# Kernel optimization log

Measured on AMD Instinct MI355X. Metric: run time of the kernel, lower is better.

The kernel has to match this reference:

```python
import jax, jax.numpy as jnp
import numpy as np

N, E, G = 20000, 160000, 64
IN_FULL, X_START, X_END = 16, 4, 10
H, OUT, RH, NE, K = 512, 512, 128, 4, 2
NL = 3               # GraphConv layers per expert
SPS, STEMP = 0.3, 1.0  # size_prior_strength, size_temperature


def setup_inputs() -> dict:
    key = jax.random.key(0)
    ks = jax.random.split(key, 10)
    def w(k, shape, fan):
        return jax.random.normal(k, shape, jnp.float32) / np.float32(np.sqrt(fan))
    return dict(
        x=jax.random.normal(ks[0], (N, IN_FULL), jnp.float32),
        edge_index=jax.random.randint(ks[1], (2, E), 0, N),
        batch=jnp.sort(jax.random.randint(ks[2], (N,), 0, G)),
        num_graphs=G,
        enc_W1=w(ks[3], (X_END - X_START, H), X_END - X_START), enc_b1=jnp.zeros((H,), jnp.float32),
        enc_W2=w(ks[4], (H, H), H), enc_b2=jnp.zeros((H,), jnp.float32),
        r_W1=w(ks[5], (H + 2, RH), H + 2), r_b1=jnp.zeros((RH,), jnp.float32),
        ln_g=jnp.ones((RH,), jnp.float32), ln_b=jnp.zeros((RH,), jnp.float32),
        r_W2=w(ks[6], (RH, NE), RH), r_b2=jnp.zeros((NE,), jnp.float32),
        size_centers=jnp.linspace(0.0, 1.0, NE).astype(jnp.float32),
        W_rel=w(ks[7], (NE, NL, H, H), H),       # GraphConv lin_rel weights (stacked)
        b_rel=jnp.zeros((NE, NL, H), jnp.float32),
        W_root=w(ks[8], (NE, NL, H, H), H),      # GraphConv lin_root weights (no bias)
    )


def reference(x, edge_index, batch, num_graphs, enc_W1, enc_b1, enc_W2, enc_b2,
              r_W1, r_b1, ln_g, ln_b, r_W2, r_b2, size_centers, W_rel, b_rel, W_root):
    src, dst = edge_index[0], edge_index[1]
    # encoder: Linear -> ReLU -> Linear on sliced node features
    h = jax.nn.relu(x[:, X_START:X_END] @ enc_W1 + enc_b1) @ enc_W2 + enc_b2
    # per-graph size features (log_nodes_edges mode)
    nodes = jnp.maximum(jax.ops.segment_sum(jnp.ones((N,), x.dtype), batch, num_segments=num_graphs), 1.0)
    edges = jax.ops.segment_sum(jnp.ones((E,), x.dtype), batch[src], num_segments=num_graphs)
    log_n, log_e = jnp.log(nodes), jnp.log1p(edges)
    f = jnp.stack([log_n, log_e], axis=-1)
    f = (f - f.mean(0, keepdims=True)) / (f.std(0, keepdims=True) + 1e-6)
    size_norm = (log_n - log_n.min()) / (log_n.max() - log_n.min() + 1e-6)
    # router: Linear -> LayerNorm -> ReLU -> Linear, plus size prior
    r = jnp.concatenate([h, f[batch]], axis=-1) @ r_W1 + r_b1
    r = (r - r.mean(-1, keepdims=True)) / jnp.sqrt(r.var(-1, keepdims=True) + 1e-5) * ln_g + ln_b
    logits = jax.nn.relu(r) @ r_W2 + r_b2
    prior = -(size_norm[batch][:, None] - size_centers[None, :]) ** 2 / STEMP
    logits = (1.0 - SPS) * logits + SPS * prior
    probs = jax.nn.softmax(logits, axis=-1)
    # top-k sparse gating, renormalized
    v, ix = jax.lax.top_k(probs, K)
    v = v / (v.sum(-1, keepdims=True) + 1e-8)
    weights = jnp.zeros_like(probs).at[jnp.arange(N)[:, None], ix].set(v)  # [N, NE]
    # GraphConv: out_i = (sum_{j->i} z_j) @ W_rel + b_rel + z_i @ W_root
    def gconv(z, Wr, br, Wo):
        agg = jax.ops.segment_sum(z[src], dst, num_segments=N)
        return agg @ Wr + br + z @ Wo
    out = jnp.zeros((N, OUT), x.dtype)
    for e in range(NE):  # small fixed expert count
        z = jax.nn.relu(gconv(h, W_rel[e, 0], b_rel[e, 0], W_root[e, 0]))
        z = jax.nn.relu(gconv(z, W_rel[e, 1], b_rel[e, 1], W_root[e, 1]))
        z = gconv(z, W_rel[e, 2], b_rel[e, 2], W_root[e, 2])
        out = out + weights[:, e:e + 1] * z
    return out
```

## Files before the change

### kernel.cpp

```cpp
#include <hip/hip_runtime.h>
#include <math.h>

#define N_NODES 20000
#define N_EDGES 160000
#define G_GRAPHS 64
#define H_DIM 512
#define RH_DIM 128
#define NE_EXP 4
#define P_ROWS 20096
#define EH_BLOCKS 64
#define WSZ (512 * 512)

typedef __attribute__((ext_vector_type(8))) short bf16x8;
typedef __attribute__((ext_vector_type(4))) float f32x4;

__device__ __forceinline__ ushort f2bf(float f) {
    uint u = __float_as_uint(f);
    return (ushort)((u + 0x7FFFu + ((u >> 16) & 1u)) >> 16);
}
__device__ __forceinline__ float bf2f(ushort h) {
    return __uint_as_float(((uint)h) << 16);
}

__device__ __forceinline__ void async_copy16(const void* g, void* l) {
    __builtin_amdgcn_global_load_lds(
        (__attribute__((address_space(1))) void*)g,
        (__attribute__((address_space(3))) void*)l, 16, 0, 0);
}

__device__ __forceinline__ int xcd_swizzle(int orig, int nwg) {
    const int q = nwg >> 3, r = nwg & 7;
    const int xcd = orig & 7, sid = orig >> 3;
    return (xcd < r ? xcd * (q + 1) : r * (q + 1) + (xcd - r) * q) + sid;
}

template<bool RELU, int EPI, int NE2>
__global__ __launch_bounds__(256)
void gemm_grp(const ushort* __restrict__ A1, size_t a1es,
              const ushort* __restrict__ W1, size_t w1es,
              const ushort* __restrict__ A2, size_t a2es,
              const ushort* __restrict__ W2, size_t w2es,
              const float* __restrict__ bias, size_t bes,
              const float* __restrict__ wcol,
              ushort* __restrict__ out0, size_t oes)
{
    __shared__ char smem[32768];
    const int tid = threadIdx.x;
    const int w = tid >> 6, lane = tid & 63;

    const int wgid = xcd_swizzle(blockIdx.x, gridDim.x);
    const int m0 = (wgid / (4 * NE2)) * 128;
    const int rem = wgid % (4 * NE2);
    const int e  = rem % NE2;
    const int n0 = (rem / NE2) * 128;

    const ushort* __restrict__ A1e = A1 + (size_t)e * a1es;
    const ushort* __restrict__ W1e = W1 + (size_t)e * w1es;
    const ushort* __restrict__ A2e = A2 + (size_t)e * a2es;
    const ushort* __restrict__ W2e = W2 + (size_t)e * w2es;
    const float*  __restrict__ be  = bias + (size_t)e * bes;
    ushort* __restrict__ oe = out0 + (size_t)e * oes;

    f32x4 acc[4][4];
#pragma unroll
    for (int i = 0; i < 4; ++i)
#pragma unroll
        for (int j = 0; j < 4; ++j) acc[i][j] = (f32x4){0.f, 0.f, 0.f, 0.f};

    const int srow = lane >> 2, schk = lane & 3;
    const int wr = w >> 1, wc = w & 1;
    const int row16 = lane & 15;
    const uint koffB = (uint)(lane >> 4) * 16u;
    const uint aoff0 = (uint)(wr * 64 + row16) * 64u + koffB;
    const uint boff0 = 8192u + (uint)(wc * 64 + row16) * 64u + koffB;

    auto stage = [&](int buf, int t) {
        const ushort* __restrict__ A  = (t < 16) ? A1e : A2e;
        const ushort* __restrict__ Wt = (t < 16) ? W1e : W2e;
        const int kt = (t & 15) * 32;
        char* base = smem + buf * 16384;
#pragma unroll
        for (int c = 0; c < 2; ++c) {
            const int rb = c * 64 + w * 16;
            async_copy16(A  + (size_t)(m0 + rb + srow) * 512 + kt + schk * 8, base + rb * 64);
            async_copy16(Wt + (size_t)(n0 + rb + srow) * 512 + kt + schk * 8, base + 8192 + rb * 64);
        }
    };
    auto compute = [&](int buf) {
        const char* base = smem + buf * 16384;
        bf16x8 af[4], bfr[4];
#pragma unroll
        for (int i = 0; i < 4; ++i) af[i] = *(const bf16x8*)(base + aoff0 + i * 1024);
#pragma unroll
        for (int j = 0; j < 4; ++j) bfr[j] = *(const bf16x8*)(base + boff0 + j * 1024);
#pragma unroll
        for (int i = 0; i < 4; ++i)
#pragma unroll
            for (int j = 0; j < 4; ++j)
                acc[i][j] = __builtin_amdgcn_mfma_f32_16x16x32_bf16(af[i], bfr[j], acc[i][j], 0, 0, 0);
    };

    stage(0, 0);
    for (int t = 0; t < 31; ++t) {
        stage((t + 1) & 1, t + 1);
        asm volatile("s_waitcnt vmcnt(4)" ::: "memory");
        __builtin_amdgcn_s_barrier();
        compute(t & 1);
        __builtin_amdgcn_s_barrier();
    }
    asm volatile("s_waitcnt vmcnt(0)" ::: "memory");
    __builtin_amdgcn_s_barrier();
    compute(1);

#pragma unroll
    for (int i = 0; i < 4; ++i) {
        const int r0 = m0 + wr * 64 + i * 16 + (lane >> 4) * 4;
#pragma unroll
        for (int j = 0; j < 4; ++j) {
            const int c = n0 + wc * 64 + j * 16 + row16;
            const float bj = be[c];
#pragma unroll
            for (int q2 = 0; q2 < 4; ++q2) {
                const int r = r0 + q2;
                float v = acc[i][j][q2] + bj;
                if (EPI == 0) {
                    if (RELU) v = fmaxf(v, 0.f);
                    oe[(size_t)r * 512 + c] = f2bf(v);
                } else {
                    const float wrow = (r < N_NODES) ? wcol[(size_t)r * 4 + e] : 0.f;
                    oe[(size_t)r * 512 + c] = f2bf(v * wrow);
                }
            }
        }
    }
}

template<int NPASS, int EPI, int NBN>
__global__ __launch_bounds__(256)
void gemm_mfma(const ushort* __restrict__ A0, const ushort* __restrict__ W0,
               const ushort* __restrict__ A1p, const ushort* __restrict__ W1p,
               const ushort* __restrict__ A2p, const ushort* __restrict__ W2p,
               const float* __restrict__ bias,
               void* __restrict__ out0, void* __restrict__ out1, int Ncols)
{
    __shared__ char smem[32768];
    const int tid = threadIdx.x;
    const int w = tid >> 6, lane = tid & 63;

    const int wgid = xcd_swizzle(blockIdx.x, gridDim.x);
    const int m0 = (wgid / NBN) * 128;
    const int n0 = (wgid % NBN) * 128;

    f32x4 acc[4][4];
#pragma unroll
    for (int i = 0; i < 4; ++i)
#pragma unroll
        for (int j = 0; j < 4; ++j) acc[i][j] = (f32x4){0.f, 0.f, 0.f, 0.f};

    const int srow = lane >> 2, schk = lane & 3;
    const int wr = w >> 1, wc = w & 1;
    const int row16 = lane & 15;
    const uint koffB = (uint)(lane >> 4) * 16u;
    const uint aoff0 = (uint)(wr * 64 + row16) * 64u + koffB;
    const uint boff0 = 8192u + (uint)(wc * 64 + row16) * 64u + koffB;

    const int NT = NPASS * 16;
    auto Asel = [&](int t) -> const ushort* { return (t < 16) ? A0 : ((t < 32) ? A1p : A2p); };
    auto Wsel = [&](int t) -> const ushort* { return (t < 16) ? W0 : ((t < 32) ? W1p : W2p); };

    auto stage = [&](int buf, int t) {
        const ushort* __restrict__ A  = Asel(t);
        const ushort* __restrict__ Wt = Wsel(t);
        const int kt = (t & 15) * 32;
        char* base = smem + buf * 16384;
#pragma unroll
        for (int c = 0; c < 2; ++c) {
            const int rb = c * 64 + w * 16;
            async_copy16(A  + (size_t)(m0 + rb + srow) * 512 + kt + schk * 8, base + rb * 64);
            async_copy16(Wt + (size_t)(n0 + rb + srow) * 512 + kt + schk * 8, base + 8192 + rb * 64);
        }
    };
    auto compute = [&](int buf) {
        const char* base = smem + buf * 16384;
        bf16x8 af[4], bfr[4];
#pragma unroll
        for (int i = 0; i < 4; ++i) af[i] = *(const bf16x8*)(base + aoff0 + i * 1024);
#pragma unroll
        for (int j = 0; j < 4; ++j) bfr[j] = *(const bf16x8*)(base + boff0 + j * 1024);
#pragma unroll
        for (int i = 0; i < 4; ++i)
#pragma unroll
            for (int j = 0; j < 4; ++j)
                acc[i][j] = __builtin_amdgcn_mfma_f32_16x16x32_bf16(af[i], bfr[j], acc[i][j], 0, 0, 0);
    };

    stage(0, 0);
    for (int t = 0; t < NT - 1; ++t) {
        stage((t + 1) & 1, t + 1);
        asm volatile("s_waitcnt vmcnt(4)" ::: "memory");
        __builtin_amdgcn_s_barrier();
        compute(t & 1);
        __builtin_amdgcn_s_barrier();
    }
    asm volatile("s_waitcnt vmcnt(0)" ::: "memory");
    __builtin_amdgcn_s_barrier();
    compute((NT - 1) & 1);

#pragma unroll
    for (int i = 0; i < 4; ++i) {
        const int r0 = m0 + wr * 64 + i * 16 + (lane >> 4) * 4;
#pragma unroll
        for (int j = 0; j < 4; ++j) {
            const int c = n0 + wc * 64 + j * 16 + row16;
            const float bj = (EPI == 5) ? 0.f : bias[c];
#pragma unroll
            for (int q2 = 0; q2 < 4; ++q2) {
                const int r = r0 + q2;
                float v = acc[i][j][q2] + bj;
                if (EPI == 4) {
                    const ushort hi = f2bf(v);
                    const ushort lo = f2bf(v - bf2f(hi));
                    ((ushort*)out0)[(size_t)r * Ncols + c] = hi;
                    ((ushort*)out1)[(size_t)r * Ncols + c] = lo;
                } else {
                    ((float*)out0)[(size_t)r * Ncols + c] = v;
                }
            }
        }
    }
}

__global__ __launch_bounds__(256)
void reduce_wz_kernel(const uint* __restrict__ wz4, float2* __restrict__ out)
{
    const size_t idx = (size_t)blockIdx.x * 256 + threadIdx.x;
    const size_t es = (size_t)P_ROWS * 256;
    const uint a = wz4[idx], b = wz4[idx + es];
    const uint c = wz4[idx + 2 * es], d = wz4[idx + 3 * es];
    float lo = bf2f((ushort)(a & 0xffffu)) + bf2f((ushort)(b & 0xffffu))
             + bf2f((ushort)(c & 0xffffu)) + bf2f((ushort)(d & 0xffffu));
    float hi = bf2f((ushort)(a >> 16)) + bf2f((ushort)(b >> 16))
             + bf2f((ushort)(c >> 16)) + bf2f((ushort)(d >> 16));
    out[idx] = make_float2(lo, hi);
}

__global__ void encoder1_kernel(const float* __restrict__ x, const float* __restrict__ W1,
                                const float* __restrict__ b1,
                                ushort* __restrict__ t1hi, ushort* __restrict__ t1lo)
{
    const int idx = blockIdx.x * blockDim.x + threadIdx.x;
    if (idx >= P_ROWS * H_DIM) return;
    const int i = idx / H_DIM, j = idx - i * H_DIM;
    float v = 0.f;
    if (i < N_NODES) {
        const float* xr = &x[i * 16 + 4];
        v = b1[j];
#pragma unroll
        for (int k = 0; k < 6; ++k) v = fmaf(xr[k], W1[k * H_DIM + j], v);
        v = fmaxf(v, 0.f);
    }
    const ushort hi = f2bf(v);
    t1hi[idx] = hi;
    t1lo[idx] = f2bf(v - bf2f(hi));
}

__global__ void zero_ints_kernel(int* __restrict__ p, int n)
{
    const int idx = blockIdx.x * blockDim.x + threadIdx.x;
    if (idx < n) p[idx] = 0;
}

__global__ void graph_bounds_kernel(const int* __restrict__ batch, int* __restrict__ gstart)
{
    const int g = threadIdx.x;
    if (g > G_GRAPHS) return;
    int lo = 0, hi = N_NODES;
    while (lo < hi) {
        const int mid = (lo + hi) >> 1;
        if (batch[mid] < g) lo = mid + 1; else hi = mid;
    }
    gstart[g] = lo;
}

__global__ __launch_bounds__(256)
void edge_hist_kernel(const int* __restrict__ src, const int* __restrict__ dst,
                      const int* __restrict__ batch,
                      int* __restrict__ part, int* __restrict__ deg)
{
    __shared__ int hist[G_GRAPHS];
    const int tid = threadIdx.x;
    if (tid < G_GRAPHS) hist[tid] = 0;
    __syncthreads();
    for (int e = blockIdx.x * 256 + tid; e < N_EDGES; e += EH_BLOCKS * 256) {
        atomicAdd(&deg[dst[e]], 1);
        atomicAdd(&hist[batch[src[e]]], 1);
    }
    __syncthreads();
    if (tid < G_GRAPHS) part[blockIdx.x * G_GRAPHS + tid] = hist[tid];
}

__global__ void stats_finalize_kernel(const int* __restrict__ gstart, const int* __restrict__ part,
                                      float* __restrict__ f_norm, float* __restrict__ size_norm)
{
    const int g = threadIdx.x;
    const float nn = fmaxf((float)(gstart[g + 1] - gstart[g]), 1.0f);
    int ec = 0;
#pragma unroll 8
    for (int b = 0; b < EH_BLOCKS; ++b) ec += part[b * G_GRAPHS + g];
    const float ee = (float)ec;
    const float ln = logf(nn);
    const float le = log1pf(ee);
    float s0 = ln, s1 = le;
#pragma unroll
    for (int o = 32; o > 0; o >>= 1) { s0 += __shfl_xor(s0, o); s1 += __shfl_xor(s1, o); }
    const float m0 = s0 / 64.f, m1 = s1 / 64.f;
    const float d0 = ln - m0, d1 = le - m1;
    float v0 = d0 * d0, v1 = d1 * d1;
#pragma unroll
    for (int o = 32; o > 0; o >>= 1) { v0 += __shfl_xor(v0, o); v1 += __shfl_xor(v1, o); }
    const float sd0 = sqrtf(v0 / 64.f), sd1 = sqrtf(v1 / 64.f);
    float mn = ln, mx = ln;
#pragma unroll
    for (int o = 32; o > 0; o >>= 1) {
        mn = fminf(mn, __shfl_xor(mn, o));
        mx = fmaxf(mx, __shfl_xor(mx, o));
    }
    f_norm[g * 2 + 0] = d0 / (sd0 + 1e-6f);
    f_norm[g * 2 + 1] = d1 / (sd1 + 1e-6f);
    size_norm[g] = (ln - mn) / (mx - mn + 1e-6f);
}

__global__ void scan_kernel(const int* __restrict__ in, int* __restrict__ row_ptr,
                            int* __restrict__ cursor, int n)
{
    __shared__ int wsum[16];
    __shared__ int carry_s;
    const int tid = threadIdx.x;
    const int lane = tid & 63, wv = tid >> 6;
    if (tid == 0) carry_s = 0;
    __syncthreads();
    for (int base = 0; base < n; base += 1024) {
        const int idx = base + tid;
        const int v = (idx < n) ? in[idx] : 0;
        int x = v;
#pragma unroll
        for (int o = 1; o < 64; o <<= 1) { const int t = __shfl_up(x, o); if (lane >= o) x += t; }
        if (lane == 63) wsum[wv] = x;
        __syncthreads();
        const int carry = carry_s;
        if (wv == 0) {
            int y = (lane < 16) ? wsum[lane] : 0;
#pragma unroll
            for (int o = 1; o < 16; o <<= 1) { const int t = __shfl_up(y, o); if (lane >= o) y += t; }
            if (lane < 16) wsum[lane] = y;
        }
        __syncthreads();
        const int woff = (wv > 0) ? wsum[wv - 1] : 0;
        const int excl = x - v + woff + carry;
        if (idx < n) { row_ptr[idx] = excl; cursor[idx] = excl; }
        __syncthreads();
        if (tid == 0) carry_s = carry + wsum[15];
        __syncthreads();
    }
    if (tid == 0) row_ptr[n] = carry_s;
}

__global__ void scatter_kernel(const int* __restrict__ src, const int* __restrict__ dst,
                               int* __restrict__ cursor, int* __restrict__ csr_col)
{
    const int e = blockIdx.x * blockDim.x + threadIdx.x;
    if (e >= N_EDGES) return;
    const int d = dst[e];
    const int slot = atomicAdd(&cursor[d], 1);
    csr_col[slot] = src[e];
}

__global__ void sort_adj_kernel(const int* __restrict__ row_ptr, int* __restrict__ csr_col)
{
    const int i = blockIdx.x * blockDim.x + threadIdx.x;
    if (i >= N_NODES) return;
    const int b = row_ptr[i], e = row_ptr[i + 1];
    for (int p = b + 1; p < e; ++p) {
        const int key = csr_col[p];
        int q = p - 1;
        while (q >= b && csr_col[q] > key) { csr_col[q + 1] = csr_col[q]; --q; }
        csr_col[q + 1] = key;
    }
}

__global__ __launch_bounds__(256)
void aggregate_bf16(const uint4* __restrict__ z4, const int* __restrict__ row_ptr,
                    const int* __restrict__ csr_col, uint4* __restrict__ agg4)
{
    const size_t es = (size_t)blockIdx.y * P_ROWS * 64;
    const uint4* __restrict__ zz = z4 + es;
    uint4* __restrict__ aa = agg4 + es;
    const int i = blockIdx.x * 4 + (threadIdx.x >> 6);
    const int lane = threadIdx.x & 63;
    const int b = row_ptr[i], e = row_ptr[i + 1];
    float acc[8];
#pragma unroll
    for (int k = 0; k < 8; ++k) acc[k] = 0.f;
    auto add8 = [&](uint4 v) {
        acc[0] += bf2f((ushort)(v.x & 0xffffu)); acc[1] += bf2f((ushort)(v.x >> 16));
        acc[2] += bf2f((ushort)(v.y & 0xffffu)); acc[3] += bf2f((ushort)(v.y >> 16));
        acc[4] += bf2f((ushort)(v.z & 0xffffu)); acc[5] += bf2f((ushort)(v.z >> 16));
        acc[6] += bf2f((ushort)(v.w & 0xffffu)); acc[7] += bf2f((ushort)(v.w >> 16));
    };
    int p = b;
    for (; p + 2 <= e; p += 2) {
        const uint4 v0 = zz[(size_t)csr_col[p] * 64 + lane];
        const uint4 v1 = zz[(size_t)csr_col[p + 1] * 64 + lane];
        add8(v0);
        add8(v1);
    }
    if (p < e) add8(zz[(size_t)csr_col[p] * 64 + lane]);
    uint4 o;
    o.x = (uint)f2bf(acc[0]) | ((uint)f2bf(acc[1]) << 16);
    o.y = (uint)f2bf(acc[2]) | ((uint)f2bf(acc[3]) << 16);
    o.z = (uint)f2bf(acc[4]) | ((uint)f2bf(acc[5]) << 16);
    o.w = (uint)f2bf(acc[6]) | ((uint)f2bf(acc[7]) << 16);
    aa[(size_t)i * 64 + lane] = o;
}

__global__ __launch_bounds__(256)
void transpose_f32_to_bf16(const float* __restrict__ W, ushort* __restrict__ Wt)
{
    __shared__ float tile[32][33];
    const float* Wm = W + (size_t)blockIdx.z * WSZ;
    ushort* Wtm = Wt + (size_t)blockIdx.z * WSZ;
    const int c0 = blockIdx.x * 32, r0 = blockIdx.y * 32;
    const int tc = threadIdx.x & 31, tr = threadIdx.x >> 5;
#pragma unroll
    for (int it = 0; it < 4; ++it)
        tile[tr + it * 8][tc] = Wm[(size_t)(r0 + tr + it * 8) * 512 + c0 + tc];
    __syncthreads();
#pragma unroll
    for (int it = 0; it < 4; ++it) {
        const int cr = tr + it * 8;
        Wtm[(size_t)(c0 + cr) * 512 + r0 + tc] = f2bf(tile[tc][cr]);
    }
}

__global__ __launch_bounds__(256)
void transpose_split_kernel(const float* __restrict__ W, ushort* __restrict__ Whi,
                            ushort* __restrict__ Wlo, int Nin)
{
    __shared__ float tile[32][33];
    const int c0 = blockIdx.x * 32;
    const int r0 = blockIdx.y * 32;
    const int tc = threadIdx.x & 31, tr = threadIdx.x >> 5;
#pragma unroll
    for (int it = 0; it < 4; ++it)
        tile[tr + it * 8][tc] = W[(size_t)(r0 + tr + it * 8) * Nin + c0 + tc];
    __syncthreads();
#pragma unroll
    for (int it = 0; it < 4; ++it) {
        const int cr = tr + it * 8;
        const float v = tile[tc][cr];
        const ushort hi = f2bf(v);
        Whi[(size_t)(c0 + cr) * 512 + r0 + tc] = hi;
        Wlo[(size_t)(c0 + cr) * 512 + r0 + tc] = f2bf(v - bf2f(hi));
    }
}

__global__ __launch_bounds__(128)
void router_kernel(const float* __restrict__ rtmp, const int* __restrict__ batch,
                   const float* __restrict__ rW1, const float* __restrict__ rb1,
                   const float* __restrict__ lng, const float* __restrict__ lnb,
                   const float* __restrict__ rW2, const float* __restrict__ rb2,
                   const float* __restrict__ centers,
                   const float* __restrict__ f_norm, const float* __restrict__ size_norm,
                   float* __restrict__ weights)
{
    const int i = blockIdx.x;
    const int j = threadIdx.x;
    const int g = batch[i];
    const float f0 = f_norm[g * 2], f1 = f_norm[g * 2 + 1];
    float r = rtmp[(size_t)i * RH_DIM + j]
            + f0 * rW1[512 * RH_DIM + j] + f1 * rW1[513 * RH_DIM + j] + rb1[j];

    __shared__ float part[2];
    __shared__ float rbuf[RH_DIM];
    __shared__ float lbuf[4];
    const int lane = j & 63, wv = j >> 6;

    float s = r;
#pragma unroll
    for (int o = 32; o > 0; o >>= 1) s += __shfl_xor(s, o);
    if (lane == 0) part[wv] = s;
    __syncthreads();
    const float mean = (part[0] + part[1]) / 128.f;
    __syncthreads();
    const float d = r - mean;
    float v = d * d;
#pragma unroll
    for (int o = 32; o > 0; o >>= 1) v += __shfl_xor(v, o);
    if (lane == 0) part[wv] = v;
    __syncthreads();
    const float var = (part[0] + part[1]) / 128.f;
    const float rn = d / sqrtf(var + 1e-5f) * lng[j] + lnb[j];
    rbuf[j] = fmaxf(rn, 0.f);
    __syncthreads();

    if (j < 4) {
        float acc = rb2[j];
        for (int t = 0; t < RH_DIM; ++t) acc = fmaf(rbuf[t], rW2[t * 4 + j], acc);
        const float sn = size_norm[g];
        const float dd = sn - centers[j];
        lbuf[j] = 0.7f * acc + 0.3f * (-(dd * dd));
    }
    __syncthreads();
    if (j == 0) {
        float p[4];
        const float mx = fmaxf(fmaxf(lbuf[0], lbuf[1]), fmaxf(lbuf[2], lbuf[3]));
#pragma unroll
        for (int c = 0; c < 4; ++c) p[c] = expf(lbuf[c] - mx);
        const float ssum = p[0] + p[1] + p[2] + p[3];
#pragma unroll
        for (int c = 0; c < 4; ++c) p[c] /= ssum;
        int i1 = 0;
#pragma unroll
        for (int c = 1; c < 4; ++c) if (p[c] > p[i1]) i1 = c;
        int i2 = -1;
#pragma unroll
        for (int c = 0; c < 4; ++c) {
            if (c == i1) continue;
            if (i2 < 0 || p[c] > p[i2]) i2 = c;
        }
        const float vs = p[i1] + p[i2] + 1e-8f;
        float wout[4] = {0.f, 0.f, 0.f, 0.f};
        wout[i1] = p[i1] / vs;
        wout[i2] = p[i2] / vs;
#pragma unroll
        for (int c = 0; c < 4; ++c) weights[(size_t)i * 4 + c] = wout[c];
    }
}

extern "C" void kernel_launch(void* const* d_in, const int* in_sizes, int n_in,
                              void* d_out, int out_size, void* d_ws, size_t ws_size,
                              hipStream_t stream)
{
    const float* x       = (const float*)d_in[0];
    const int*   ei      = (const int*)d_in[1];
    const int*   batch   = (const int*)d_in[2];
    const float* enc_W1  = (const float*)d_in[4];
    const float* enc_b1  = (const float*)d_in[5];
    const float* enc_W2  = (const float*)d_in[6];
    const float* enc_b2  = (const float*)d_in[7];
    const float* r_W1    = (const float*)d_in[8];
    const float* r_b1    = (const float*)d_in[9];
    const float* ln_g    = (const float*)d_in[10];
    const float* ln_b    = (const float*)d_in[11];
    const float* r_W2    = (const float*)d_in[12];
    const float* r_b2    = (const float*)d_in[13];
    const float* centers = (const float*)d_in[14];
    const float* W_rel   = (const float*)d_in[15];
    const float* b_rel   = (const float*)d_in[16];
    const float* W_root  = (const float*)d_in[17];
    const int* src = ei;
    const int* dst = ei + N_EDGES;
    float* out = (float*)d_out;

    const size_t PF = (size_t)P_ROWS * H_DIM;
    const size_t PF2 = PF * 2;

    char* wsp = (char*)d_ws;
    size_t off = 0;
    auto alloc = [&](size_t bytes) -> char* {
        char* p = wsp + off;
        off = (off + bytes + 255) & ~(size_t)255;
        return p;
    };
    char* region1 = alloc(PF * 4);
    ushort* t1hi = (ushort*)region1;
    ushort* t1lo = (ushort*)(region1 + PF * 2);
    ushort* wz4  = (ushort*)region1;
    char* region2 = alloc(PF * 4);
    ushort* h_hi = (ushort*)region2;
    ushort* h_lo = (ushort*)(region2 + PF * 2);
    char* B_zA = alloc(PF2 * 2);
    ushort* zAe = (ushort*)B_zA;
    float*  rtmp = (float*)B_zA;
    char* B_zB = alloc(PF2 * 2);
    ushort* zBe = (ushort*)B_zB;
    char* B_ag = alloc(PF2 * 2);
    ushort* agge = (ushort*)B_ag;
    ushort* aggH16 = (ushort*)alloc(PF * 2);
    ushort* Wt_rel16  = (ushort*)alloc((size_t)12 * WSZ * 2);
    ushort* Wt_root16 = (ushort*)alloc((size_t)12 * WSZ * 2);
    ushort* W2t_hi = (ushort*)alloc((size_t)WSZ * 2);
    ushort* W2t_lo = (ushort*)alloc((size_t)WSZ * 2);
    ushort* rW1t_hi = (ushort*)alloc((size_t)128 * 512 * 2);
    ushort* rW1t_lo = (ushort*)alloc((size_t)128 * 512 * 2);
    float*  weights = (float*)alloc((size_t)P_ROWS * 4 * 4);
    int* deg     = (int*)alloc((size_t)N_NODES * 4);
    int* gstart  = (int*)alloc((size_t)(G_GRAPHS + 1) * 4);
    int* part    = (int*)alloc((size_t)EH_BLOCKS * G_GRAPHS * 4);
    int* row_ptr = (int*)alloc((size_t)(N_NODES + 1) * 4);
    int* cursor  = (int*)alloc((size_t)N_NODES * 4);
    int* csr_col = (int*)alloc((size_t)N_EDGES * 4);
    float* f_norm    = (float*)alloc((size_t)G_GRAPHS * 2 * 4);
    float* size_norm = (float*)alloc((size_t)G_GRAPHS * 4);
    (void)in_sizes; (void)n_in; (void)out_size; (void)ws_size;

    const int enc_nwg  = 4 * (P_ROWS / 128);
    const int rtr_nwg  = 1 * (P_ROWS / 128);
    const int grp_nwg2 = 8 * (P_ROWS / 128);
    const dim3 tr_grid(16, 16, 12);
    const dim3 agg_grid1(N_NODES / 4, 1);
    const dim3 agg_grid2(N_NODES / 4, 2);

    zero_ints_kernel<<<(N_NODES + 255) / 256, 256, 0, stream>>>(deg, N_NODES);
    transpose_f32_to_bf16<<<tr_grid, 256, 0, stream>>>(W_rel, Wt_rel16);
    transpose_f32_to_bf16<<<tr_grid, 256, 0, stream>>>(W_root, Wt_root16);
    transpose_split_kernel<<<dim3(16, 16), 256, 0, stream>>>(enc_W2, W2t_hi, W2t_lo, 512);
    transpose_split_kernel<<<dim3(4, 16), 256, 0, stream>>>(r_W1, rW1t_hi, rW1t_lo, 128);
    graph_bounds_kernel<<<1, 128, 0, stream>>>(batch, gstart);
    edge_hist_kernel<<<EH_BLOCKS, 256, 0, stream>>>(src, dst, batch, part, deg);
    stats_finalize_kernel<<<1, 64, 0, stream>>>(gstart, part, f_norm, size_norm);
    encoder1_kernel<<<(P_ROWS * H_DIM + 255) / 256, 256, 0, stream>>>(x, enc_W1, enc_b1, t1hi, t1lo);
    gemm_mfma<3, 4, 4><<<enc_nwg, 256, 0, stream>>>(
        t1hi, W2t_hi, t1hi, W2t_lo, t1lo, W2t_hi, enc_b2, h_hi, h_lo, 512);
    gemm_mfma<3, 5, 1><<<rtr_nwg, 256, 0, stream>>>(
        h_hi, rW1t_hi, h_hi, rW1t_lo, h_lo, rW1t_hi, nullptr, rtmp, nullptr, 128);
    router_kernel<<<N_NODES, 128, 0, stream>>>(rtmp, batch, r_W1, r_b1, ln_g, ln_b,
                                               r_W2, r_b2, centers, f_norm, size_norm, weights);
    scan_kernel<<<1, 1024, 0, stream>>>(deg, row_ptr, cursor, N_NODES);
    scatter_kernel<<<(N_EDGES + 255) / 256, 256, 0, stream>>>(src, dst, cursor, csr_col);
    sort_adj_kernel<<<(N_NODES + 255) / 256, 256, 0, stream>>>(row_ptr, csr_col);
    aggregate_bf16<<<agg_grid1, 256, 0, stream>>>((const uint4*)h_hi, row_ptr, csr_col,
                                                  (uint4*)aggH16);

    const size_t WES = (size_t)3 * WSZ;
    const size_t BES = (size_t)3 * 512;
    for (int p = 0; p < 2; ++p) {
        const size_t eb = (size_t)(p * 2);
        const ushort* WrP = Wt_rel16  + eb * WES;
        const ushort* WoP = Wt_root16 + eb * WES;
        const float*  brP = b_rel + eb * BES;
        ushort* wzP = wz4 + eb * PF;
        gemm_grp<true, 0, 2><<<grp_nwg2, 256, 0, stream>>>(
            aggH16, 0, WrP, WES, h_hi, 0, WoP, WES, brP, BES, nullptr, zAe, PF);
        aggregate_bf16<<<agg_grid2, 256, 0, stream>>>((const uint4*)zAe, row_ptr, csr_col,
                                                      (uint4*)agge);
        gemm_grp<true, 0, 2><<<grp_nwg2, 256, 0, stream>>>(
            agge, PF, WrP + WSZ, WES, zAe, PF, WoP + WSZ, WES, brP + 512, BES, nullptr, zBe, PF);
        aggregate_bf16<<<agg_grid2, 256, 0, stream>>>((const uint4*)zBe, row_ptr, csr_col,
                                                      (uint4*)agge);
        gemm_grp<false, 6, 2><<<grp_nwg2, 256, 0, stream>>>(
            agge, PF, WrP + 2 * WSZ, WES, zBe, PF, WoP + 2 * WSZ, WES, brP + 1024, BES,
            weights + eb, wzP, PF);
    }
    reduce_wz_kernel<<<N_NODES, 256, 0, stream>>>((const uint*)wz4, (float2*)out);
}
```

Baseline: 837.5 us.

## Compute last GraphConv layer only for rows routed to each expert

```diff
diff --git a/kernel.cpp b/kernel.cpp
--- a/kernel.cpp
+++ b/kernel.cpp
@@ -34,14 +34,13 @@
     return (xcd < r ? xcd * (q + 1) : r * (q + 1) + (xcd - r) * q) + sid;
 }
 
-template<bool RELU, int EPI, int NE2>
+template<bool RELU, int NE2>
 __global__ __launch_bounds__(256)
 void gemm_grp(const ushort* __restrict__ A1, size_t a1es,
               const ushort* __restrict__ W1, size_t w1es,
               const ushort* __restrict__ A2, size_t a2es,
               const ushort* __restrict__ W2, size_t w2es,
               const float* __restrict__ bias, size_t bes,
-              const float* __restrict__ wcol,
               ushort* __restrict__ out0, size_t oes)
 {
     __shared__ char smem[32768];
@@ -121,15 +120,120 @@
             const float bj = be[c];
 #pragma unroll
             for (int q2 = 0; q2 < 4; ++q2) {
-                const int r = r0 + q2;
                 float v = acc[i][j][q2] + bj;
-                if (EPI == 0) {
-                    if (RELU) v = fmaxf(v, 0.f);
-                    oe[(size_t)r * 512 + c] = f2bf(v);
-                } else {
-                    const float wrow = (r < N_NODES) ? wcol[(size_t)r * 4 + e] : 0.f;
-                    oe[(size_t)r * 512 + c] = f2bf(v * wrow);
-                }
+                if (RELU) v = fmaxf(v, 0.f);
+                oe[(size_t)(r0 + q2) * 512 + c] = f2bf(v);
+            }
+        }
+    }
+}
+
+__global__ __launch_bounds__(256)
+void gemm_l2(const ushort* __restrict__ A1, size_t a1es,
+             const ushort* __restrict__ W1, size_t w1es,
+             const ushort* __restrict__ A2, size_t a2es,
+             const ushort* __restrict__ W2, size_t w2es,
+             const float* __restrict__ bias, size_t bes,
+             const float* __restrict__ weights4,
+             const int* __restrict__ lists, const int* __restrict__ cnt8,
+             int egbase, ushort* __restrict__ planes)
+{
+    __shared__ char smem[32768];
+    const int tid = threadIdx.x;
+    const int w = tid >> 6, lane = tid & 63;
+
+    const int wgid = xcd_swizzle(blockIdx.x, gridDim.x);
+    const int m0 = (wgid / 16) * 128;
+    const int rem = wgid % 16;
+    const int li = rem & 3;
+    const int n0 = (rem >> 2) * 128;
+    const int el = li >> 1, pl = li & 1;
+    const int eg = egbase + el;
+    const int lid = eg * 2 + pl;
+    const int cnt = cnt8[lid];
+    if (m0 >= cnt) return;
+    const int* __restrict__ idxl = lists + (size_t)lid * N_NODES;
+
+    const ushort* __restrict__ A1e = A1 + (size_t)el * a1es;
+    const ushort* __restrict__ W1e = W1 + (size_t)el * w1es;
+    const ushort* __restrict__ A2e = A2 + (size_t)el * a2es;
+    const ushort* __restrict__ W2e = W2 + (size_t)el * w2es;
+    const float*  __restrict__ be  = bias + (size_t)el * bes;
+
+    f32x4 acc[4][4];
+#pragma unroll
+    for (int i = 0; i < 4; ++i)
+#pragma unroll
+        for (int j = 0; j < 4; ++j) acc[i][j] = (f32x4){0.f, 0.f, 0.f, 0.f};
+
+    const int srow = lane >> 2, schk = lane & 3;
+    const int wr = w >> 1, wc = w & 1;
+    const int row16 = lane & 15;
+    const uint koffB = (uint)(lane >> 4) * 16u;
+    const uint aoff0 = (uint)(wr * 64 + row16) * 64u + koffB;
+    const uint boff0 = 8192u + (uint)(wc * 64 + row16) * 64u + koffB;
+
+    size_t arow[2];
+#pragma unroll
+    for (int c = 0; c < 2; ++c) {
+        int slot = m0 + c * 64 + w * 16 + srow;
+        slot = (slot < cnt) ? slot : (cnt - 1);
+        arow[c] = (size_t)idxl[slot] * 512 + schk * 8;
+    }
+
+    auto stage = [&](int buf, int t) {
+        const ushort* __restrict__ A  = (t < 16) ? A1e : A2e;
+        const ushort* __restrict__ Wt = (t < 16) ? W1e : W2e;
+        const int kt = (t & 15) * 32;
+        char* base = smem + buf * 16384;
+#pragma unroll
+        for (int c = 0; c < 2; ++c) {
+            const int rb = c * 64 + w * 16;
+            async_copy16(A + arow[c] + kt, base + rb * 64);
+            async_copy16(Wt + (size_t)(n0 + rb + srow) * 512 + kt + schk * 8, base + 8192 + rb * 64);
+        }
+    };
+    auto compute = [&](int buf) {
+        const char* base = smem + buf * 16384;
+        bf16x8 af[4], bfr[4];
+#pragma unroll
+        for (int i = 0; i < 4; ++i) af[i] = *(const bf16x8*)(base + aoff0 + i * 1024);
+#pragma unroll
+        for (int j = 0; j < 4; ++j) bfr[j] = *(const bf16x8*)(base + boff0 + j * 1024);
+#pragma unroll
+        for (int i = 0; i < 4; ++i)
+#pragma unroll
+            for (int j = 0; j < 4; ++j)
+                acc[i][j] = __builtin_amdgcn_mfma_f32_16x16x32_bf16(af[i], bfr[j], acc[i][j], 0, 0, 0);
+    };
+
+    stage(0, 0);
+    for (int t = 0; t < 31; ++t) {
+        stage((t + 1) & 1, t + 1);
+        asm volatile("s_waitcnt vmcnt(4)" ::: "memory");
+        __builtin_amdgcn_s_barrier();
+        compute(t & 1);
+        __builtin_amdgcn_s_barrier();
+    }
+    asm volatile("s_waitcnt vmcnt(0)" ::: "memory");
+    __builtin_amdgcn_s_barrier();
+    compute(1);
+
+    ushort* __restrict__ plane = planes + (size_t)pl * ((size_t)P_ROWS * H_DIM);
+#pragma unroll
+    for (int i = 0; i < 4; ++i) {
+        const int s0 = m0 + wr * 64 + i * 16 + (lane >> 4) * 4;
+#pragma unroll
+        for (int q2 = 0; q2 < 4; ++q2) {
+            const int s = s0 + q2;
+            if (s >= cnt) continue;
+            const int r = idxl[s];
+            const float wrow = weights4[(size_t)r * 4 + eg];
+#pragma unroll
+            for (int j = 0; j < 4; ++j) {
+                const int c = n0 + wc * 64 + j * 16 + row16;
+                const float v = acc[i][j][q2] + be[c];
+                plane[(size_t)r * 512 + c] = f2bf(v * wrow);
             }
         }
     }
@@ -231,17 +335,44 @@
 }
 
 __global__ __launch_bounds__(256)
-void reduce_wz_kernel(const uint* __restrict__ wz4, float2* __restrict__ out)
+void reduce2_kernel(const uint* __restrict__ p0, const uint* __restrict__ p1,
+                    float2* __restrict__ out)
 {
     const size_t idx = (size_t)blockIdx.x * 256 + threadIdx.x;
-    const size_t es = (size_t)P_ROWS * 256;
-    const uint a = wz4[idx], b = wz4[idx + es];
-    const uint c = wz4[idx + 2 * es], d = wz4[idx + 3 * es];
-    float lo = bf2f((ushort)(a & 0xffffu)) + bf2f((ushort)(b & 0xffffu))
-             + bf2f((ushort)(c & 0xffffu)) + bf2f((ushort)(d & 0xffffu));
-    float hi = bf2f((ushort)(a >> 16)) + bf2f((ushort)(b >> 16))
-             + bf2f((ushort)(c >> 16)) + bf2f((ushort)(d >> 16));
+    const uint a = p0[idx], b = p1[idx];
+    float lo = bf2f((ushort)(a & 0xffffu)) + bf2f((ushort)(b & 0xffffu));
+    float hi = bf2f((ushort)(a >> 16)) + bf2f((ushort)(b >> 16));
     out[idx] = make_float2(lo, hi);
+}
+
+__global__ __launch_bounds__(256)
+void select_kernel(const float* __restrict__ weights, int* __restrict__ cnt8,
+                   int* __restrict__ lists)
+{
+    __shared__ int lcnt[8];
+    __shared__ int lbase[8];
+    const int tid = threadIdx.x;
+    if (tid < 8) lcnt[tid] = 0;
+    __syncthreads();
+    const int r = blockIdx.x * 256 + tid;
+    int e1 = -1, e2 = -1, s1 = 0, s2 = 0;
+    if (r < N_NODES) {
+#pragma unroll
+        for (int c = 0; c < 4; ++c) {
+            if (weights[(size_t)r * 4 + c] > 0.f) {
+                if (e1 < 0) e1 = c; else e2 = c;
+            }
+        }
+        s1 = atomicAdd(&lcnt[e1 * 2 + 0], 1);
+        s2 = atomicAdd(&lcnt[e2 * 2 + 1], 1);
+    }
+    __syncthreads();
+    if (tid < 8) lbase[tid] = atomicAdd(&cnt8[tid], lcnt[tid]);
+    __syncthreads();
+    if (r < N_NODES) {
+        lists[(size_t)(e1 * 2 + 0) * N_NODES + lbase[e1 * 2 + 0] + s1] = r;
+        lists[(size_t)(e2 * 2 + 1) * N_NODES + lbase[e2 * 2 + 1] + s2] = r;
+    }
 }
 
 __global__ void encoder1_kernel(const float* __restrict__ x, const float* __restrict__ W1,
@@ -575,7 +706,7 @@
     char* region1 = alloc(PF * 4);
     ushort* t1hi = (ushort*)region1;
     ushort* t1lo = (ushort*)(region1 + PF * 2);
-    ushort* wz4  = (ushort*)region1;
+    ushort* planes = (ushort*)region1;
     char* region2 = alloc(PF * 4);
     ushort* h_hi = (ushort*)region2;
     ushort* h_lo = (ushort*)(region2 + PF * 2);
@@ -594,12 +725,14 @@
     ushort* rW1t_hi = (ushort*)alloc((size_t)128 * 512 * 2);
     ushort* rW1t_lo = (ushort*)alloc((size_t)128 * 512 * 2);
     float*  weights = (float*)alloc((size_t)P_ROWS * 4 * 4);
-    int* deg     = (int*)alloc((size_t)N_NODES * 4);
+    int* deg     = (int*)alloc((size_t)(N_NODES + 8) * 4);
+    int* cnt8    = deg + N_NODES;
     int* gstart  = (int*)alloc((size_t)(G_GRAPHS + 1) * 4);
     int* part    = (int*)alloc((size_t)EH_BLOCKS * G_GRAPHS * 4);
     int* row_ptr = (int*)alloc((size_t)(N_NODES + 1) * 4);
     int* cursor  = (int*)alloc((size_t)N_NODES * 4);
     int* csr_col = (int*)alloc((size_t)N_EDGES * 4);
+    int* lists   = (int*)alloc((size_t)8 * N_NODES * 4);
     float* f_norm    = (float*)alloc((size_t)G_GRAPHS * 2 * 4);
     float* size_norm = (float*)alloc((size_t)G_GRAPHS * 4);
     (void)in_sizes; (void)n_in; (void)out_size; (void)ws_size;
@@ -607,11 +740,12 @@
     const int enc_nwg  = 4 * (P_ROWS / 128);
     const int rtr_nwg  = 1 * (P_ROWS / 128);
     const int grp_nwg2 = 8 * (P_ROWS / 128);
+    const int l2_nwg   = 16 * (P_ROWS / 128);
     const dim3 tr_grid(16, 16, 12);
     const dim3 agg_grid1(N_NODES / 4, 1);
     const dim3 agg_grid2(N_NODES / 4, 2);
 
-    zero_ints_kernel<<<(N_NODES + 255) / 256, 256, 0, stream>>>(deg, N_NODES);
+    zero_ints_kernel<<<(N_NODES + 8 + 255) / 256, 256, 0, stream>>>(deg, N_NODES + 8);
     transpose_f32_to_bf16<<<tr_grid, 256, 0, stream>>>(W_rel, Wt_rel16);
     transpose_f32_to_bf16<<<tr_grid, 256, 0, stream>>>(W_root, Wt_root16);
     transpose_split_kernel<<<dim3(16, 16), 256, 0, stream>>>(enc_W2, W2t_hi, W2t_lo, 512);
@@ -626,6 +760,7 @@
         h_hi, rW1t_hi, h_hi, rW1t_lo, h_lo, rW1t_hi, nullptr, rtmp, nullptr, 128);
     router_kernel<<<N_NODES, 128, 0, stream>>>(rtmp, batch, r_W1, r_b1, ln_g, ln_b,
                                                r_W2, r_b2, centers, f_norm, size_norm, weights);
+    select_kernel<<<(N_NODES + 255) / 256, 256, 0, stream>>>(weights, cnt8, lists);
     scan_kernel<<<1, 1024, 0, stream>>>(deg, row_ptr, cursor, N_NODES);
     scatter_kernel<<<(N_EDGES + 255) / 256, 256, 0, stream>>>(src, dst, cursor, csr_col);
     sort_adj_kernel<<<(N_NODES + 255) / 256, 256, 0, stream>>>(row_ptr, csr_col);
@@ -639,18 +774,18 @@
         const ushort* WrP = Wt_rel16  + eb * WES;
         const ushort* WoP = Wt_root16 + eb * WES;
         const float*  brP = b_rel + eb * BES;
-        ushort* wzP = wz4 + eb * PF;
-        gemm_grp<true, 0, 2><<<grp_nwg2, 256, 0, stream>>>(
-            aggH16, 0, WrP, WES, h_hi, 0, WoP, WES, brP, BES, nullptr, zAe, PF);
+        gemm_grp<true, 2><<<grp_nwg2, 256, 0, stream>>>(
+            aggH16, 0, WrP, WES, h_hi, 0, WoP, WES, brP, BES, zAe, PF);
         aggregate_bf16<<<agg_grid2, 256, 0, stream>>>((const uint4*)zAe, row_ptr, csr_col,
                                                       (uint4*)agge);
-        gemm_grp<true, 0, 2><<<grp_nwg2, 256, 0, stream>>>(
-            agge, PF, WrP + WSZ, WES, zAe, PF, WoP + WSZ, WES, brP + 512, BES, nullptr, zBe, PF);
+        gemm_grp<true, 2><<<grp_nwg2, 256, 0, stream>>>(
+            agge, PF, WrP + WSZ, WES, zAe, PF, WoP + WSZ, WES, brP + 512, BES, zBe, PF);
         aggregate_bf16<<<agg_grid2, 256, 0, stream>>>((const uint4*)zBe, row_ptr, csr_col,
                                                       (uint4*)agge);
-        gemm_grp<false, 6, 2><<<grp_nwg2, 256, 0, stream>>>(
+        gemm_l2<<<l2_nwg, 256, 0, stream>>>(
             agge, PF, WrP + 2 * WSZ, WES, zBe, PF, WoP + 2 * WSZ, WES, brP + 1024, BES,
-            weights + eb, wzP, PF);
-    }
-    reduce_wz_kernel<<<N_NODES, 256, 0, stream>>>((const uint*)wz4, (float2*)out);
-}
+            weights, lists, cnt8, (int)eb, planes);
+    }
+    reduce2_kernel<<<N_NODES, 256, 0, stream>>>((const uint*)planes,
+                                                (const uint*)(planes + PF), (float2*)out);
+}
```

Result: slower. 914.6 us (+9.2%).
